# Performance work log

Hardware: AMD Instinct MI355X
Metric: run time of the kernel (lower is better)

## Reference

```python
import jax, jax.numpy as jnp
import numpy as np

BN_EPS = 1e-5


def _weight_mlp(off, Wh, bh, Wo, bo):
    # off: [Nout, k, 2] relative neighbor offsets -> [Nout, k, 9] interp coeffs
    h = jax.nn.relu(off @ Wh + bh)
    return h @ Wo + bo


def _interp_conv(x, idx, off, Wk, bk, Wh, bh, Wo, bo):
    # x: [B, Cin, Nin]; idx: [Nout, k] neighbor indices into Nin; Wk: [Cout, Cin, 9]
    a = _weight_mlp(off, Wh, bh, Wo, bo)        # [Nout, k, 9]
    feats = x[:, :, idx]                         # gather -> [B, Cin, Nout, k]
    # dynamic filter: per-neighbor kernel = a @ Wk taps, contracted with features
    y = jnp.einsum('nkt,bcnk,oct->bon', a, feats, Wk)  # [B, Cout, Nout]
    return y + bk[None, :, None]


def _bn_relu(x, g, b):
    # BatchNorm1d over [B, C, N] using batch statistics (training-mode forward)
    mean = x.mean(axis=(0, 2), keepdims=True)
    var = x.var(axis=(0, 2), keepdims=True)
    xn = (x - mean) * jax.lax.rsqrt(var + BN_EPS)
    return jax.nn.relu(xn * g[None, :, None] + b[None, :, None])


def setup_inputs() -> dict:
    key = jax.random.key(0)
    ks = jax.random.split(key, 12)
    B, N1, N2, N3, K = 8, 50176, 12544, 3136, 9
    inp = {
        'x': jax.random.normal(ks[0], (B, 3, N1), jnp.float32),
        'nbr1': jax.random.randint(ks[1], (N2, K), 0, N1, jnp.int32),
        'off1': jax.random.normal(ks[2], (N2, K, 2), jnp.float32),
        'nbr2': jax.random.randint(ks[3], (N2, K), 0, N2, jnp.int32),
        'off2': jax.random.normal(ks[4], (N2, K, 2), jnp.float32),
        'pool_idx': jax.random.randint(ks[5], (N3, K), 0, N2, jnp.int32),
        'Wh': jax.random.normal(ks[6], (2, 32), jnp.float32) * 0.5,
        'bh': jnp.zeros((32,), jnp.float32),
        'Wo': jax.random.normal(ks[7], (32, 9), jnp.float32) * 0.2,
        'bo': jnp.zeros((9,), jnp.float32),
        'W1': jax.random.normal(ks[8], (32, 3, 9), jnp.float32) * 0.2,
        'b1': jnp.zeros((32,), jnp.float32),
        'W2': jax.random.normal(ks[9], (32, 32, 9), jnp.float32) * 0.06,
        'b2': jnp.zeros((32,), jnp.float32),
        'W3': jax.random.normal(ks[10], (64, 32, 9), jnp.float32) * 0.06,
        'b3': jnp.zeros((64,), jnp.float32),
        'g1': jnp.ones((32,), jnp.float32), 'be1': jnp.zeros((32,), jnp.float32),
        'g2': jnp.ones((32,), jnp.float32), 'be2': jnp.zeros((32,), jnp.float32),
        'g3': jnp.ones((64,), jnp.float32), 'be3': jnp.zeros((64,), jnp.float32),
    }
    return inp


def reference(x, nbr1, off1, nbr2, off2, pool_idx, Wh, bh, Wo, bo,
              W1, b1, W2, b2, W3, b3, g1, be1, g2, be2, g3, be3):
    x = _bn_relu(_interp_conv(x, nbr1, off1, W1, b1, Wh, bh, Wo, bo), g1, be1)
    x = _bn_relu(_interp_conv(x, nbr2, off2, W2, b2, Wh, bh, Wo, bo), g2, be2)
    x = _bn_relu(_interp_conv(x, nbr2, off2, W3, b3, Wh, bh, Wo, bo), g3, be3)
    # MaxPoolNG: max over irregular neighbor sets from level l2 -> l3
    x = x[:, :, pool_idx].max(axis=-1)           # [B, 64, N3]
    return x
```

## Files before the change

kernel.cpp:

```cpp
#include <hip/hip_runtime.h>
#include <math.h>

#define N1C 50176
#define N2C 12544
#define N3C 3136
#define NT_TILES (N2C * 8 / 64)

typedef __attribute__((ext_vector_type(8))) short bf16x8;
typedef __attribute__((ext_vector_type(4))) float f32x4;

__device__ __forceinline__ unsigned short f2bf(float f) {
    unsigned u = __builtin_bit_cast(unsigned, f);
    u += 0x7fffu + ((u >> 16) & 1u);
    return (unsigned short)(u >> 16);
}
__device__ __forceinline__ unsigned packbf(float a, float b) {
    return (unsigned)f2bf(a) | ((unsigned)f2bf(b) << 16);
}
__device__ __forceinline__ float bf2f(unsigned short u) {
    return __builtin_bit_cast(float, (unsigned)u << 16);
}
__device__ __forceinline__ float bflo(unsigned u) {
    return __builtin_bit_cast(float, u << 16);
}
__device__ __forceinline__ float bfhi(unsigned u) {
    return __builtin_bit_cast(float, u & 0xffff0000u);
}

#define TRB (N1C / 64)
#define MLB (2 * N2C * 9 / 256)
#define PWB 112

__device__ __forceinline__ void pad_one(int i, const float* __restrict__ W,
                                        unsigned short* __restrict__ Wp,
                                        int OC, int CIN, int KT) {
    int j = i & 7;
    int op = (i >> 3) & 31;
    int q = (i >> 8) & 3;
    int kt = (i >> 10) % KT;
    int g = i / (KT * 1024);
    int kp = kt * 32 + q * 8 + j;
    int t = kp / CIN, c = kp - t * CIN;
    int o = g * 32 + op;
    float v = (t < 9 && o < OC) ? W[(o * CIN + c) * 9 + t] : 0.f;
    Wp[i] = f2bf(v);
}

__global__ void prologue_kernel(const float* __restrict__ x, unsigned short* __restrict__ X0,
                                const float* __restrict__ off1, const float* __restrict__ off2,
                                const float* __restrict__ Wh, const float* __restrict__ bh,
                                const float* __restrict__ Wo, const float* __restrict__ bo,
                                float* __restrict__ A1, float* __restrict__ A2,
                                const float* __restrict__ W1, const float* __restrict__ W2,
                                const float* __restrict__ W3,
                                unsigned short* __restrict__ W1p, unsigned short* __restrict__ W2p,
                                unsigned short* __restrict__ W3p) {
    __shared__ float T[64][25];
    int blk = blockIdx.x;
    int tid = threadIdx.x;
    if (blk < TRB) {
        int n0 = blk * 64;
        for (int r = tid; r < 24 * 64; r += 256) {
            int cb = r >> 6;
            int nn = r & 63;
            T[nn][cb] = x[cb * N1C + n0 + nn];
        }
        __syncthreads();
        for (int w = tid; w < 64 * 24; w += 256) {
            int nn = w / 24;
            int u = w - nn * 24;
            X0[(n0 + nn) * 24 + u] = f2bf(T[nn][u]);
        }
    } else if (blk < TRB + MLB) {
        int idx = (blk - TRB) * 256 + tid;
        const float* offp;
        float* Ap;
        if (idx < N2C * 9) { offp = off1 + idx * 2; Ap = A1 + idx * 9; }
        else { int i2 = idx - N2C * 9; offp = off2 + i2 * 2; Ap = A2 + i2 * 9; }
        float o0 = offp[0], o1 = offp[1];
        float out[9];
#pragma unroll
        for (int t = 0; t < 9; t++) out[t] = bo[t];
#pragma unroll
        for (int h = 0; h < 32; h++) {
            float hv = fmaxf(o0 * Wh[h] + o1 * Wh[32 + h] + bh[h], 0.f);
#pragma unroll
            for (int t = 0; t < 9; t++) out[t] += hv * Wo[h * 9 + t];
        }
#pragma unroll
        for (int t = 0; t < 9; t++) Ap[t] = out[t];
    } else {
        int i = (blk - TRB - MLB) * 256 + tid;
        if (i < 1024) pad_one(i, W1, W1p, 32, 3, 1);
        else if (i < 10240) pad_one(i - 1024, W2, W2p, 32, 32, 9);
        else pad_one(i - 10240, W3, W3p, 64, 32, 9);
    }
}

template <int CIN, int MW, bool HAS_BN>
__global__ __launch_bounds__(256, 4)
void conv_kernel(const unsigned short* __restrict__ Xin,
                 const int* __restrict__ nbr,
                 const float* __restrict__ A,
                 const unsigned short* __restrict__ Wp,
                 const float* __restrict__ bias,
                 const float* __restrict__ bnsc,
                 const float* __restrict__ bnsh,
                 unsigned short* __restrict__ Yb,
                 double* __restrict__ Part) {
    constexpr int OC = MW * 16;
    constexpr int KREAL = 9 * CIN;
    constexpr int KROW = (KREAL + 31) & ~31;
    constexpr int KT = KROW / 32;
    constexpr int KSTR = KROW + 8;
    __shared__ alignas(16) short S[64 * KSTR];

    int tid = threadIdx.x;
    int tile = blockIdx.x;
    int n0 = tile * 8;

    if constexpr (KROW != KREAL) {
        for (int i = tid; i < 64 * KSTR; i += 256) S[i] = 0;
        __syncthreads();
    }

    if constexpr (CIN == 3) {
        if (tid < 192) {
            int nsub = tid / 24;
            int u = tid - nsub * 24;
            int b = u / 3, c = u - b * 3;
            int n = n0 + nsub;
            const int* nb = nbr + n * 9;
            const float* Ar = A + n * 81;
            float s[9];
#pragma unroll
            for (int t = 0; t < 9; t++) s[t] = 0.f;
#pragma unroll
            for (int k = 0; k < 9; k++) {
                float f = bf2f(Xin[nb[k] * 24 + u]);
#pragma unroll
                for (int t = 0; t < 9; t++) s[t] = fmaf(Ar[k * 9 + t], f, s[t]);
            }
            int col = nsub * 8 + b;
#pragma unroll
            for (int t = 0; t < 9; t++) S[col * KSTR + t * 3 + c] = (short)f2bf(s[t]);
        }
    } else {
        int nhalf = __builtin_amdgcn_readfirstlane(tid >> 7);
        int rem = tid & 127;
        int b = rem >> 4, c2 = rem & 15;
        float sc0 = 1.f, sh0 = 0.f, sc1 = 1.f, sh1 = 0.f;
        if (HAS_BN) {
            sc0 = bnsc[2 * c2];     sc1 = bnsc[2 * c2 + 1];
            sh0 = bnsh[2 * c2];     sh1 = bnsh[2 * c2 + 1];
        }
        const unsigned* Xu = (const unsigned*)Xin;
        int nbase = n0 + nhalf * 4;
        unsigned fu[36];
#pragma unroll
        for (int g = 0; g < 4; g++)
#pragma unroll
            for (int k = 0; k < 9; k++) {
                int j = nbr[(nbase + g) * 9 + k];
                fu[g * 9 + k] = Xu[(size_t)j * 128 + rem];
            }
#pragma unroll
        for (int g = 0; g < 4; g++) {
            const float* Ar = A + (nbase + g) * 81;
            float s0[9], s1[9];
#pragma unroll
            for (int t = 0; t < 9; t++) { s0[t] = 0.f; s1[t] = 0.f; }
#pragma unroll
            for (int k = 0; k < 9; k++) {
                unsigned u = fu[g * 9 + k];
                float lo = bflo(u), hi = bfhi(u);
                if (HAS_BN) {
                    lo = fmaxf(fmaf(lo, sc0, sh0), 0.f);
                    hi = fmaxf(fmaf(hi, sc1, sh1), 0.f);
                }
#pragma unroll
                for (int t = 0; t < 9; t++) {
                    float a = Ar[k * 9 + t];
                    s0[t] = fmaf(a, lo, s0[t]);
                    s1[t] = fmaf(a, hi, s1[t]);
                }
            }
            int col = (nhalf * 4 + g) * 8 + b;
            unsigned* Srow = (unsigned*)&S[col * KSTR];
#pragma unroll
            for (int t = 0; t < 9; t++) Srow[t * 16 + c2] = packbf(s0[t], s1[t]);
        }
    }
    __syncthreads();

    int lane = tid & 63, wv = tid >> 6, q = lane >> 4, cl = lane & 15;
    int colg = wv * 16 + cl;

    const bf16x8* wf = (const bf16x8*)Wp;
    f32x4 acc[MW];
#pragma unroll
    for (int m = 0; m < MW; m++) acc[m] = (f32x4){0.f, 0.f, 0.f, 0.f};
#pragma unroll
    for (int kt = 0; kt < KT; kt++) {
        bf16x8 bfr = *(const bf16x8*)&S[colg * KSTR + kt * 32 + q * 8];
#pragma unroll
        for (int m = 0; m < MW; m++) {
            const bf16x8* wg = wf + (m >> 1) * (KT * 128);
            bf16x8 am = wg[(kt * 4 + q) * 32 + cl + (m & 1) * 16];
            acc[m] = __builtin_amdgcn_mfma_f32_16x16x32_bf16(am, bfr, acc[m], 0, 0, 0);
        }
    }
    __syncthreads();
    double (*redd)[2 * OC] = (double(*)[2 * OC])S;

    int C = tile * 64 + colg;
    float yv[4 * MW];
#pragma unroll
    for (int m = 0; m < MW; m++)
#pragma unroll
        for (int i = 0; i < 4; i++) {
            int o = m * 16 + q * 4 + i;
            float y = acc[m][i] + bias[o];
            yv[m * 4 + i] = y;
            Yb[(size_t)C * OC + o] = f2bf(y);
        }
#pragma unroll
    for (int r = 0; r < 4 * MW; r++) {
        double ps = (double)yv[r];
        double pq = (double)yv[r] * (double)yv[r];
#pragma unroll
        for (int d = 1; d < 16; d <<= 1) {
            ps += __shfl_xor(ps, d);
            pq += __shfl_xor(pq, d);
        }
        if (cl == 0) {
            int o = (r >> 2) * 16 + q * 4 + (r & 3);
            redd[wv][o] = ps;
            redd[wv][OC + o] = pq;
        }
    }
    __syncthreads();
    if (tid < 2 * OC) {
        double v = redd[0][tid] + redd[1][tid] + redd[2][tid] + redd[3][tid];
        Part[(size_t)tid * NT_TILES + tile] = v;
    }
}

__global__ __launch_bounds__(256, 8)
void bn_reduce(const double* __restrict__ Part,
               const float* __restrict__ g, const float* __restrict__ be,
               float* __restrict__ sc, float* __restrict__ sh, int OC) {
    int o = blockIdx.x;
    int tid = threadIdx.x;
    const double* ps = Part + (size_t)o * NT_TILES;
    const double* pq = Part + (size_t)(OC + o) * NT_TILES;
    double s = 0.0, q = 0.0;
    for (int t = tid; t < NT_TILES; t += 256) {
        s += ps[t];
        q += pq[t];
    }
#pragma unroll
    for (int d = 1; d < 64; d <<= 1) {
        s += __shfl_xor(s, d);
        q += __shfl_xor(q, d);
    }
    __shared__ double red[8];
    int wv = tid >> 6;
    if ((tid & 63) == 0) { red[wv] = s; red[4 + wv] = q; }
    __syncthreads();
    if (tid == 0) {
        double S = red[0] + red[1] + red[2] + red[3];
        double Q = red[4] + red[5] + red[6] + red[7];
        double cnt = (double)N2C * 8.0;
        double mean = S / cnt;
        double var = Q / cnt - mean * mean;
        double rs = 1.0 / sqrt(var + 1e-5);
        double scale = (double)g[o] * rs;
        sc[o] = (float)scale;
        sh[o] = (float)((double)be[o] - mean * scale);
    }
}

__global__ __launch_bounds__(512, 4)
void pool_kernel(const unsigned short* __restrict__ Y3, const int* __restrict__ pidx,
                 const float* __restrict__ sc, const float* __restrict__ sh,
                 float* __restrict__ out) {
    int m0 = blockIdx.x * 8;
    int tid = threadIdx.x;
    int o = tid & 63;
    float s = sc[o], h = sh[o];
    float mx[8];
    int jn[9];
#pragma unroll
    for (int k = 0; k < 9; k++) jn[k] = pidx[m0 * 9 + k];
#pragma unroll 1
    for (int mi = 0; mi < 8; mi++) {
        int jc[9];
#pragma unroll
        for (int k = 0; k < 9; k++) jc[k] = jn[k];
        if (mi < 7) {
#pragma unroll
            for (int k = 0; k < 9; k++) jn[k] = pidx[(m0 + mi + 1) * 9 + k];
        }
        float v0 = 0.f;
#pragma unroll
        for (int k = 0; k < 9; k++) {
            float v = bf2f(Y3[(size_t)jc[k] * 512 + tid]);
            v0 = fmaxf(v0, fmaf(v, s, h));
        }
        mx[mi] = fmaxf(v0, 0.f);
    }
    float* op = out + (size_t)tid * 3136 + m0;
#pragma unroll
    for (int mi = 0; mi < 8; mi++) op[mi] = mx[mi];
}

extern "C" void kernel_launch(void* const* d_in, const int* in_sizes, int n_in,
                              void* d_out, int out_size, void* d_ws, size_t ws_size,
                              hipStream_t stream) {
    const float* x    = (const float*)d_in[0];
    const int*   nbr1 = (const int*)d_in[1];
    const float* off1 = (const float*)d_in[2];
    const int*   nbr2 = (const int*)d_in[3];
    const float* off2 = (const float*)d_in[4];
    const int*   pidx = (const int*)d_in[5];
    const float* Wh   = (const float*)d_in[6];
    const float* bh   = (const float*)d_in[7];
    const float* Wo   = (const float*)d_in[8];
    const float* bo   = (const float*)d_in[9];
    const float* W1   = (const float*)d_in[10];
    const float* b1   = (const float*)d_in[11];
    const float* W2   = (const float*)d_in[12];
    const float* b2   = (const float*)d_in[13];
    const float* W3   = (const float*)d_in[14];
    const float* b3   = (const float*)d_in[15];
    const float* g1   = (const float*)d_in[16];
    const float* be1  = (const float*)d_in[17];
    const float* g2   = (const float*)d_in[18];
    const float* be2  = (const float*)d_in[19];
    const float* g3   = (const float*)d_in[20];
    const float* be3  = (const float*)d_in[21];

    char* ws = (char*)d_ws;
    size_t off = 0;
    auto alloc = [&](size_t bytes) -> void* {
        void* p = ws + off;
        off += (bytes + 255) & ~(size_t)255;
        return p;
    };
    unsigned short* X0b = (unsigned short*)alloc((size_t)N1C * 24 * 2);
    float* A1 = (float*)alloc((size_t)N2C * 81 * 4);
    float* A2 = (float*)alloc((size_t)N2C * 81 * 4);
    unsigned short* Y1b = (unsigned short*)alloc((size_t)N2C * 8 * 32 * 2);
    unsigned short* Y2b = (unsigned short*)alloc((size_t)N2C * 8 * 32 * 2);
    unsigned short* Y3b = (unsigned short*)alloc((size_t)N2C * 8 * 64 * 2);
    unsigned short* W1p = (unsigned short*)alloc(32 * 32 * 2);
    unsigned short* W2p = (unsigned short*)alloc(32 * 288 * 2);
    unsigned short* W3p = (unsigned short*)alloc(64 * 288 * 2);
    double* Part  = (double*)alloc((size_t)NT_TILES * 128 * 8);
    float*  scbuf = (float*)alloc(256 * 4);

    float* sc1 = scbuf;       float* sh1 = scbuf + 32;
    float* sc2 = scbuf + 64;  float* sh2 = scbuf + 96;
    float* sc3 = scbuf + 128; float* sh3 = scbuf + 192;

    prologue_kernel<<<TRB + MLB + PWB, 256, 0, stream>>>(
        x, X0b, off1, off2, Wh, bh, Wo, bo, A1, A2, W1, W2, W3, W1p, W2p, W3p);

    conv_kernel<3, 2, false><<<NT_TILES, 256, 0, stream>>>(
        X0b, nbr1, A1, W1p, b1, nullptr, nullptr, Y1b, Part);
    bn_reduce<<<32, 256, 0, stream>>>(Part, g1, be1, sc1, sh1, 32);

    conv_kernel<32, 2, true><<<NT_TILES, 256, 0, stream>>>(
        Y1b, nbr2, A2, W2p, b2, sc1, sh1, Y2b, Part);
    bn_reduce<<<32, 256, 0, stream>>>(Part, g2, be2, sc2, sh2, 32);

    conv_kernel<32, 4, true><<<NT_TILES, 256, 0, stream>>>(
        Y2b, nbr2, A2, W3p, b3, sc2, sh2, Y3b, Part);
    bn_reduce<<<64, 256, 0, stream>>>(Part, g3, be3, sc3, sh3, 64);

    pool_kernel<<<N3C / 8, 512, 0, stream>>>(Y3b, pidx, sc3, sh3, (float*)d_out);
}
```

Before: 217.3 us.

## Split BN stats into separate pass and pipeline two tiles per conv block

BatchNorm statistics are no longer reduced inside the conv kernels; a new bn_sum kernel re-reads the bf16 outputs and accumulates per-channel sums in double over 128 blocks, and bn_fin finalizes them. The 32-channel conv kernels now process two tiles per block, issuing the gather for the second tile before the MFMA stage of the first so load latency overlaps compute. Outputs are also written as packed 8-byte vectors instead of scalar bf16 stores. The cost is an extra full read of each activation tensor and statistics computed from bf16-rounded values rather than fp32.

```diff
diff --git a/kernel.cpp b/kernel.cpp
--- a/kernel.cpp
+++ b/kernel.cpp
@@ -8,6 +8,7 @@
 
 typedef __attribute__((ext_vector_type(8))) short bf16x8;
 typedef __attribute__((ext_vector_type(4))) float f32x4;
+typedef __attribute__((ext_vector_type(2))) unsigned uint2v;
 
 __device__ __forceinline__ unsigned short f2bf(float f) {
     unsigned u = __builtin_bit_cast(unsigned, f);
@@ -97,105 +98,14 @@
     }
 }
 
-template <int CIN, int MW, bool HAS_BN>
-__global__ __launch_bounds__(256, 4)
-void conv_kernel(const unsigned short* __restrict__ Xin,
-                 const int* __restrict__ nbr,
-                 const float* __restrict__ A,
-                 const unsigned short* __restrict__ Wp,
-                 const float* __restrict__ bias,
-                 const float* __restrict__ bnsc,
-                 const float* __restrict__ bnsh,
-                 unsigned short* __restrict__ Yb,
-                 double* __restrict__ Part) {
+template <int MW, int KT, int KSTR>
+__device__ __forceinline__ void mfmaStore(const short* S, const unsigned short* Wp,
+                                          const float* __restrict__ bias,
+                                          unsigned short* __restrict__ Yb,
+                                          int tile, int tid) {
     constexpr int OC = MW * 16;
-    constexpr int KREAL = 9 * CIN;
-    constexpr int KROW = (KREAL + 31) & ~31;
-    constexpr int KT = KROW / 32;
-    constexpr int KSTR = KROW + 8;
-    __shared__ alignas(16) short S[64 * KSTR];
-
-    int tid = threadIdx.x;
-    int tile = blockIdx.x;
-    int n0 = tile * 8;
-
-    if constexpr (KROW != KREAL) {
-        for (int i = tid; i < 64 * KSTR; i += 256) S[i] = 0;
-        __syncthreads();
-    }
-
-    if constexpr (CIN == 3) {
-        if (tid < 192) {
-            int nsub = tid / 24;
-            int u = tid - nsub * 24;
-            int b = u / 3, c = u - b * 3;
-            int n = n0 + nsub;
-            const int* nb = nbr + n * 9;
-            const float* Ar = A + n * 81;
-            float s[9];
-#pragma unroll
-            for (int t = 0; t < 9; t++) s[t] = 0.f;
-#pragma unroll
-            for (int k = 0; k < 9; k++) {
-                float f = bf2f(Xin[nb[k] * 24 + u]);
-#pragma unroll
-                for (int t = 0; t < 9; t++) s[t] = fmaf(Ar[k * 9 + t], f, s[t]);
-            }
-            int col = nsub * 8 + b;
-#pragma unroll
-            for (int t = 0; t < 9; t++) S[col * KSTR + t * 3 + c] = (short)f2bf(s[t]);
-        }
-    } else {
-        int nhalf = __builtin_amdgcn_readfirstlane(tid >> 7);
-        int rem = tid & 127;
-        int b = rem >> 4, c2 = rem & 15;
-        float sc0 = 1.f, sh0 = 0.f, sc1 = 1.f, sh1 = 0.f;
-        if (HAS_BN) {
-            sc0 = bnsc[2 * c2];     sc1 = bnsc[2 * c2 + 1];
-            sh0 = bnsh[2 * c2];     sh1 = bnsh[2 * c2 + 1];
-        }
-        const unsigned* Xu = (const unsigned*)Xin;
-        int nbase = n0 + nhalf * 4;
-        unsigned fu[36];
-#pragma unroll
-        for (int g = 0; g < 4; g++)
-#pragma unroll
-            for (int k = 0; k < 9; k++) {
-                int j = nbr[(nbase + g) * 9 + k];
-                fu[g * 9 + k] = Xu[(size_t)j * 128 + rem];
-            }
-#pragma unroll
-        for (int g = 0; g < 4; g++) {
-            const float* Ar = A + (nbase + g) * 81;
-            float s0[9], s1[9];
-#pragma unroll
-            for (int t = 0; t < 9; t++) { s0[t] = 0.f; s1[t] = 0.f; }
-#pragma unroll
-            for (int k = 0; k < 9; k++) {
-                unsigned u = fu[g * 9 + k];
-                float lo = bflo(u), hi = bfhi(u);
-                if (HAS_BN) {
-                    lo = fmaxf(fmaf(lo, sc0, sh0), 0.f);
-                    hi = fmaxf(fmaf(hi, sc1, sh1), 0.f);
-                }
-#pragma unroll
-                for (int t = 0; t < 9; t++) {
-                    float a = Ar[k * 9 + t];
-                    s0[t] = fmaf(a, lo, s0[t]);
-                    s1[t] = fmaf(a, hi, s1[t]);
-                }
-            }
-            int col = (nhalf * 4 + g) * 8 + b;
-            unsigned* Srow = (unsigned*)&S[col * KSTR];
-#pragma unroll
-            for (int t = 0; t < 9; t++) Srow[t * 16 + c2] = packbf(s0[t], s1[t]);
-        }
-    }
-    __syncthreads();
-
     int lane = tid & 63, wv = tid >> 6, q = lane >> 4, cl = lane & 15;
     int colg = wv * 16 + cl;
-
     const bf16x8* wf = (const bf16x8*)Wp;
     f32x4 acc[MW];
 #pragma unroll
@@ -210,70 +120,196 @@
             acc[m] = __builtin_amdgcn_mfma_f32_16x16x32_bf16(am, bfr, acc[m], 0, 0, 0);
         }
     }
-    __syncthreads();
-    double (*redd)[2 * OC] = (double(*)[2 * OC])S;
-
     int C = tile * 64 + colg;
-    float yv[4 * MW];
-#pragma unroll
-    for (int m = 0; m < MW; m++)
-#pragma unroll
-        for (int i = 0; i < 4; i++) {
-            int o = m * 16 + q * 4 + i;
-            float y = acc[m][i] + bias[o];
-            yv[m * 4 + i] = y;
-            Yb[(size_t)C * OC + o] = f2bf(y);
-        }
-#pragma unroll
-    for (int r = 0; r < 4 * MW; r++) {
-        double ps = (double)yv[r];
-        double pq = (double)yv[r] * (double)yv[r];
-#pragma unroll
-        for (int d = 1; d < 16; d <<= 1) {
-            ps += __shfl_xor(ps, d);
-            pq += __shfl_xor(pq, d);
-        }
-        if (cl == 0) {
-            int o = (r >> 2) * 16 + q * 4 + (r & 3);
-            redd[wv][o] = ps;
-            redd[wv][OC + o] = pq;
-        }
+#pragma unroll
+    for (int m = 0; m < MW; m++) {
+        int ob = m * 16 + q * 4;
+        float y0 = acc[m][0] + bias[ob + 0];
+        float y1 = acc[m][1] + bias[ob + 1];
+        float y2 = acc[m][2] + bias[ob + 2];
+        float y3 = acc[m][3] + bias[ob + 3];
+        uint2v uu;
+        uu.x = packbf(y0, y1);
+        uu.y = packbf(y2, y3);
+        *(uint2v*)&Yb[(size_t)C * OC + ob] = uu;
+    }
+}
+
+__global__ __launch_bounds__(256, 4)
+void conv1_kernel(const unsigned short* __restrict__ Xin,
+                  const int* __restrict__ nbr,
+                  const float* __restrict__ A,
+                  const unsigned short* __restrict__ Wp,
+                  const float* __restrict__ bias,
+                  unsigned short* __restrict__ Yb) {
+    constexpr int KSTR = 40;
+    __shared__ alignas(16) short S[64 * KSTR];
+    int tid = threadIdx.x;
+    int n0 = blockIdx.x * 8;
+    for (int i = tid; i < 64 * KSTR; i += 256) S[i] = 0;
+    __syncthreads();
+    if (tid < 192) {
+        int nsub = tid / 24;
+        int u = tid - nsub * 24;
+        int b = u / 3, c = u - b * 3;
+        int n = n0 + nsub;
+        const int* nb = nbr + n * 9;
+        const float* Ar = A + n * 81;
+        float f[9];
+#pragma unroll
+        for (int k = 0; k < 9; k++) f[k] = bf2f(Xin[nb[k] * 24 + u]);
+        float s[9];
+#pragma unroll
+        for (int t = 0; t < 9; t++) s[t] = 0.f;
+#pragma unroll
+        for (int k = 0; k < 9; k++)
+#pragma unroll
+            for (int t = 0; t < 9; t++) s[t] = fmaf(Ar[k * 9 + t], f[k], s[t]);
+        int col = nsub * 8 + b;
+#pragma unroll
+        for (int t = 0; t < 9; t++) S[col * KSTR + t * 3 + c] = (short)f2bf(s[t]);
+    }
+    __syncthreads();
+    mfmaStore<2, 1, KSTR>(S, Wp, bias, Yb, blockIdx.x, tid);
+}
+
+#define KSTR32 296
+
+__device__ __forceinline__ void gather36(unsigned* fu, const unsigned* __restrict__ Xu,
+                                         const int* __restrict__ nbr, int nbase, int rem) {
+#pragma unroll
+    for (int g = 0; g < 4; g++)
+#pragma unroll
+        for (int k = 0; k < 9; k++) {
+            int j = nbr[(nbase + g) * 9 + k];
+            fu[g * 9 + k] = Xu[(size_t)j * 128 + rem];
+        }
+}
+
+template <bool HAS_BN>
+__device__ __forceinline__ void phaseA32(const unsigned* fu, const float* __restrict__ A,
+                                         int nbase, short* S, int nhalf, int b, int c2,
+                                         float sc0, float sh0, float sc1, float sh1) {
+#pragma unroll
+    for (int g = 0; g < 4; g++) {
+        const float* Ar = A + (nbase + g) * 81;
+        float s0[9], s1[9];
+#pragma unroll
+        for (int t = 0; t < 9; t++) { s0[t] = 0.f; s1[t] = 0.f; }
+#pragma unroll
+        for (int k = 0; k < 9; k++) {
+            unsigned u = fu[g * 9 + k];
+            float lo = bflo(u), hi = bfhi(u);
+            if (HAS_BN) {
+                lo = fmaxf(fmaf(lo, sc0, sh0), 0.f);
+                hi = fmaxf(fmaf(hi, sc1, sh1), 0.f);
+            }
+#pragma unroll
+            for (int t = 0; t < 9; t++) {
+                float a = Ar[k * 9 + t];
+                s0[t] = fmaf(a, lo, s0[t]);
+                s1[t] = fmaf(a, hi, s1[t]);
+            }
+        }
+        int col = (nhalf * 4 + g) * 8 + b;
+        unsigned* Srow = (unsigned*)&S[col * KSTR32];
+#pragma unroll
+        for (int t = 0; t < 9; t++) Srow[t * 16 + c2] = packbf(s0[t], s1[t]);
+    }
+}
+
+template <int MW, bool HAS_BN>
+__global__ __launch_bounds__(256, 4)
+void conv32_kernel(const unsigned short* __restrict__ Xin,
+                   const int* __restrict__ nbr,
+                   const float* __restrict__ A,
+                   const unsigned short* __restrict__ Wp,
+                   const float* __restrict__ bias,
+                   const float* __restrict__ bnsc,
+                   const float* __restrict__ bnsh,
+                   unsigned short* __restrict__ Yb) {
+    __shared__ alignas(16) short S[64 * KSTR32];
+    int tid = threadIdx.x;
+    int nhalf = __builtin_amdgcn_readfirstlane(tid >> 7);
+    int rem = tid & 127;
+    int b = rem >> 4, c2 = rem & 15;
+    float sc0 = 1.f, sh0 = 0.f, sc1 = 1.f, sh1 = 0.f;
+    if (HAS_BN) {
+        sc0 = bnsc[2 * c2]; sc1 = bnsc[2 * c2 + 1];
+        sh0 = bnsh[2 * c2]; sh1 = bnsh[2 * c2 + 1];
+    }
+    const unsigned* Xu = (const unsigned*)Xin;
+    int tile0 = blockIdx.x * 2;
+    int tile1 = tile0 + 1;
+    int nb0 = tile0 * 8 + nhalf * 4;
+    int nb1 = tile1 * 8 + nhalf * 4;
+
+    unsigned fu[36];
+    gather36(fu, Xu, nbr, nb0, rem);
+    phaseA32<HAS_BN>(fu, A, nb0, S, nhalf, b, c2, sc0, sh0, sc1, sh1);
+    __syncthreads();
+
+    unsigned fu2[36];
+    gather36(fu2, Xu, nbr, nb1, rem);
+    mfmaStore<MW, 9, KSTR32>(S, Wp, bias, Yb, tile0, tid);
+    __syncthreads();
+
+    phaseA32<HAS_BN>(fu2, A, nb1, S, nhalf, b, c2, sc0, sh0, sc1, sh1);
+    __syncthreads();
+    mfmaStore<MW, 9, KSTR32>(S, Wp, bias, Yb, tile1, tid);
+}
+
+template <int OC>
+__global__ __launch_bounds__(256, 8)
+void bn_sum(const unsigned short* __restrict__ Yb, double* __restrict__ Part) {
+    constexpr int CLS = OC / 2;
+    constexpr int TOTU = N2C * 8 * OC / 2;
+    const unsigned* Yu = (const unsigned*)Yb;
+    int tid = threadIdx.x;
+    double s0 = 0, q0 = 0, s1 = 0, q1 = 0;
+    for (int p = blockIdx.x * 256 + tid; p < TOTU; p += 128 * 256) {
+        unsigned u = Yu[p];
+        double lo = (double)bflo(u), hi = (double)bfhi(u);
+        s0 += lo; q0 += lo * lo;
+        s1 += hi; q1 += hi * hi;
+    }
+#pragma unroll
+    for (int d = CLS; d < 64; d <<= 1) {
+        s0 += __shfl_xor(s0, d); q0 += __shfl_xor(q0, d);
+        s1 += __shfl_xor(s1, d); q1 += __shfl_xor(q1, d);
+    }
+    __shared__ double red[4][CLS][4];
+    int wv = tid >> 6, lane = tid & 63;
+    if (lane < CLS) {
+        red[wv][lane][0] = s0; red[wv][lane][1] = q0;
+        red[wv][lane][2] = s1; red[wv][lane][3] = q1;
     }
     __syncthreads();
     if (tid < 2 * OC) {
-        double v = redd[0][tid] + redd[1][tid] + redd[2][tid] + redd[3][tid];
-        Part[(size_t)tid * NT_TILES + tile] = v;
-    }
-}
-
-__global__ __launch_bounds__(256, 8)
-void bn_reduce(const double* __restrict__ Part,
-               const float* __restrict__ g, const float* __restrict__ be,
-               float* __restrict__ sc, float* __restrict__ sh, int OC) {
+        int o = (tid < OC) ? tid : tid - OC;
+        int isq = (tid >= OC) ? 1 : 0;
+        int cls = o >> 1, slot = (o & 1) * 2 + isq;
+        double v = red[0][cls][slot] + red[1][cls][slot] + red[2][cls][slot] + red[3][cls][slot];
+        Part[(size_t)tid * 128 + blockIdx.x] = v;
+    }
+}
+
+__global__ void bn_fin(const double* __restrict__ Part,
+                       const float* __restrict__ g, const float* __restrict__ be,
+                       float* __restrict__ sc, float* __restrict__ sh, int OC) {
     int o = blockIdx.x;
-    int tid = threadIdx.x;
-    const double* ps = Part + (size_t)o * NT_TILES;
-    const double* pq = Part + (size_t)(OC + o) * NT_TILES;
-    double s = 0.0, q = 0.0;
-    for (int t = tid; t < NT_TILES; t += 256) {
-        s += ps[t];
-        q += pq[t];
-    }
+    int t = threadIdx.x;
+    double s = Part[(size_t)o * 128 + t] + Part[(size_t)o * 128 + t + 64];
+    double q = Part[(size_t)(OC + o) * 128 + t] + Part[(size_t)(OC + o) * 128 + t + 64];
 #pragma unroll
     for (int d = 1; d < 64; d <<= 1) {
         s += __shfl_xor(s, d);
         q += __shfl_xor(q, d);
     }
-    __shared__ double red[8];
-    int wv = tid >> 6;
-    if ((tid & 63) == 0) { red[wv] = s; red[4 + wv] = q; }
-    __syncthreads();
-    if (tid == 0) {
-        double S = red[0] + red[1] + red[2] + red[3];
-        double Q = red[4] + red[5] + red[6] + red[7];
+    if (t == 0) {
         double cnt = (double)N2C * 8.0;
-        double mean = S / cnt;
-        double var = Q / cnt - mean * mean;
+        double mean = s / cnt;
+        double var = q / cnt - mean * mean;
         double rs = 1.0 / sqrt(var + 1e-5);
         double scale = (double)g[o] * rs;
         sc[o] = (float)scale;
@@ -357,7 +393,7 @@
     unsigned short* W1p = (unsigned short*)alloc(32 * 32 * 2);
     unsigned short* W2p = (unsigned short*)alloc(32 * 288 * 2);
     unsigned short* W3p = (unsigned short*)alloc(64 * 288 * 2);
-    double* Part  = (double*)alloc((size_t)NT_TILES * 128 * 8);
+    double* Part  = (double*)alloc(128 * 128 * 8);
     float*  scbuf = (float*)alloc(256 * 4);
 
     float* sc1 = scbuf;       float* sh1 = scbuf + 32;
@@ -367,17 +403,19 @@
     prologue_kernel<<<TRB + MLB + PWB, 256, 0, stream>>>(
         x, X0b, off1, off2, Wh, bh, Wo, bo, A1, A2, W1, W2, W3, W1p, W2p, W3p);
 
-    conv_kernel<3, 2, false><<<NT_TILES, 256, 0, stream>>>(
-        X0b, nbr1, A1, W1p, b1, nullptr, nullptr, Y1b, Part);
-    bn_reduce<<<32, 256, 0, stream>>>(Part, g1, be1, sc1, sh1, 32);
-
-    conv_kernel<32, 2, true><<<NT_TILES, 256, 0, stream>>>(
-        Y1b, nbr2, A2, W2p, b2, sc1, sh1, Y2b, Part);
-    bn_reduce<<<32, 256, 0, stream>>>(Part, g2, be2, sc2, sh2, 32);
-
-    conv_kernel<32, 4, true><<<NT_TILES, 256, 0, stream>>>(
-        Y2b, nbr2, A2, W3p, b3, sc2, sh2, Y3b, Part);
-    bn_reduce<<<64, 256, 0, stream>>>(Part, g3, be3, sc3, sh3, 64);
+    conv1_kernel<<<NT_TILES, 256, 0, stream>>>(X0b, nbr1, A1, W1p, b1, Y1b);
+    bn_sum<32><<<128, 256, 0, stream>>>(Y1b, Part);
+    bn_fin<<<32, 64, 0, stream>>>(Part, g1, be1, sc1, sh1, 32);
+
+    conv32_kernel<2, true><<<NT_TILES / 2, 256, 0, stream>>>(
+        Y1b, nbr2, A2, W2p, b2, sc1, sh1, Y2b);
+    bn_sum<32><<<128, 256, 0, stream>>>(Y2b, Part);
+    bn_fin<<<32, 64, 0, stream>>>(Part, g2, be2, sc2, sh2, 32);
+
+    conv32_kernel<4, true><<<NT_TILES / 2, 256, 0, stream>>>(
+        Y2b, nbr2, A2, W3p, b3, sc2, sh2, Y3b);
+    bn_sum<64><<<128, 256, 0, stream>>>(Y3b, Part);
+    bn_fin<<<64, 64, 0, stream>>>(Part, g3, be3, sc3, sh3, 64);
 
     pool_kernel<<<N3C / 8, 512, 0, stream>>>(Y3b, pidx, sc3, sh3, (float*)d_out);
 }
```

After: 240.6 us. 10.8% more time.
